# Optimization experiments

Hardware: AMD Instinct MI355X
Metric: run time of the kernel (lower is better)

The kernel has to match this reference:

```python
import jax, jax.numpy as jnp
import numpy as np

N_NODES = 100000
IN_FEATURES = 5000
OUT_FEATURES = 64
NNZ = 4000000


def setup_inputs() -> dict:
    key = jax.random.key(0)
    k_row, k_col, k_val, k_w, k_b = jax.random.split(key, 5)
    rows = jax.random.randint(k_row, (NNZ,), 0, N_NODES, dtype=jnp.int64 if jax.config.jax_enable_x64 else jnp.int32)
    cols = jax.random.randint(k_col, (NNZ,), 0, IN_FEATURES, dtype=rows.dtype)
    index = jnp.stack([rows, cols], axis=0)  # [2, nnz] COO
    value = jax.random.uniform(k_val, (NNZ,), dtype=jnp.float32)
    # kaiming_uniform_(mode='fan_out', a=sqrt(5)) on [in, out]: fan_out = out_features
    gain = np.sqrt(2.0 / (1.0 + 5.0))
    bound_w = gain * np.sqrt(3.0 / OUT_FEATURES)
    weight = jax.random.uniform(k_w, (IN_FEATURES, OUT_FEATURES), jnp.float32, -bound_w, bound_w)
    bound_b = 1.0 / np.sqrt(OUT_FEATURES)
    bias = jax.random.uniform(k_b, (OUT_FEATURES,), jnp.float32, -bound_b, bound_b)
    return {"index": index, "value": value, "n": N_NODES, "weight": weight, "bias": bias}


def reference(index, value, n, weight, bias):
    # spmm: out[r, :] = sum over nnz with row==r of value * weight[col, :]
    rows, cols = index[0], index[1]
    contrib = value[:, None] * weight[cols]            # [nnz, out] gather + scale
    res = jax.ops.segment_sum(contrib, rows, num_segments=n)  # [n, out] scatter-add
    return res + bias[None, :]
```

## Files before the change

kernel.cpp:

```cpp
#include <hip/hip_runtime.h>


#define NBF 1024
#define DMAX 128
#define CH 4096
#define CC 1536
#define SP_T 512

__global__ void k_zero1024(int* __restrict__ p) { p[threadIdx.x] = 0; }

__global__ __launch_bounds__(512) void kA_hist(const int* __restrict__ rows, int nnz,
        unsigned M, int S, int* __restrict__ hist2dF, int* __restrict__ hist2dC) {
    __shared__ int h[NBF];
    int t = threadIdx.x, blk = blockIdx.x;
    long long base = (long long)blk * CH;
    int count = (int)min((long long)CH, (long long)nnz - base);
    h[t] = 0; h[t + 512] = 0;
    __syncthreads();
#pragma unroll
    for (int k = 0; k < 8; ++k) {
        int i = t + (k << 9);
        if (i < count) {
            unsigned r = (unsigned)rows[base + i];
            int f = (int)(((unsigned long long)r * M) >> S);
            atomicAdd(&h[f], 1);
        }
    }
    __syncthreads();
    hist2dF[blk * NBF + t] = h[t];
    hist2dF[blk * NBF + 512 + t] = h[t + 512];
    if (t < 64) {
        int s = 0;
#pragma unroll
        for (int j = 0; j < 16; ++j) s += h[(t << 4) + j];
        hist2dC[(blk << 6) + t] = s;
    }
}

__global__ __launch_bounds__(1024) void kB1_reduce(const int* __restrict__ hist2dF,
        int nChunks, int* __restrict__ gcnt) {
    int t = threadIdx.x;
    int s = 0;
    for (int b = blockIdx.x; b < nChunks; b += gridDim.x) s += hist2dF[b * NBF + t];
    if (s) atomicAdd(&gcnt[t], s);
}

__global__ __launch_bounds__(1024) void kB_off(const int* __restrict__ gcnt,
        const int* __restrict__ hist2dC, int nChunks, int* __restrict__ fineBase,
        int* __restrict__ cursorF, int* __restrict__ blockOffC, int doOff) {
    __shared__ int sE[NBF];
    __shared__ int wsum[16];
    __shared__ int totalSh;
    int t = threadIdx.x, lane = t & 63, wv = t >> 6;
    int v = gcnt[t];
    int x = v;
#pragma unroll
    for (int off = 1; off < 64; off <<= 1) {
        int y = __shfl_up(x, off, 64);
        if (lane >= off) x += y;
    }
    if (lane == 63) wsum[wv] = x;
    __syncthreads();
    if (t < 16) {
        int s = wsum[t], xs = s;
#pragma unroll
        for (int off = 1; off < 16; off <<= 1) {
            int y = __shfl_up(xs, off, 16);
            if (t >= off) xs += y;
        }
        wsum[t] = xs - s;
    }
    __syncthreads();
    int incl = x + wsum[wv], excl = incl - v;
    sE[t] = excl;
    if (blockIdx.x == 0) {
        fineBase[t] = excl;
        cursorF[t] = excl;
        if (t == NBF - 1) fineBase[NBF] = incl;
    }
    __syncthreads();
    if (!doOff) return;
    int c = blockIdx.x;
    int carry = sE[c << 4];
    for (int b2 = 0; b2 < nChunks; b2 += 1024) {
        int idx = b2 + t;
        int hv = (idx < nChunks) ? hist2dC[(idx << 6) + c] : 0;
        int hx = hv;
#pragma unroll
        for (int off = 1; off < 64; off <<= 1) {
            int y = __shfl_up(hx, off, 64);
            if (lane >= off) hx += y;
        }
        if (lane == 63) wsum[wv] = hx;
        __syncthreads();
        if (t < 16) {
            int s = wsum[t], xs = s;
#pragma unroll
            for (int off = 1; off < 16; off <<= 1) {
                int y = __shfl_up(xs, off, 16);
                if (t >= off) xs += y;
            }
            wsum[t] = xs - s;
        }
        __syncthreads();
        int hincl = hx + wsum[wv];
        if (idx < nChunks) blockOffC[(idx << 6) + c] = carry + hincl - hv;
        if (t == 1023) totalSh = hincl;
        __syncthreads();
        carry += totalSh;
    }
}

__global__ void k_ghist(const int* __restrict__ rows, int nnz, unsigned M, int S,
                        int* __restrict__ gcnt) {
    __shared__ int h[NBF];
    int t = threadIdx.x;
    for (int i = t; i < NBF; i += blockDim.x) h[i] = 0;
    __syncthreads();
    for (int i = blockIdx.x * blockDim.x + t; i < nnz; i += gridDim.x * blockDim.x) {
        unsigned r = (unsigned)rows[i];
        int f = (int)(((unsigned long long)r * M) >> S);
        atomicAdd(&h[f], 1);
    }
    __syncthreads();
    for (int i = t; i < NBF; i += blockDim.x)
        if (h[i]) atomicAdd(&gcnt[i], h[i]);
}

__global__ __launch_bounds__(512) void kC_bin1(const int* __restrict__ rows,
        const int* __restrict__ cols, const float* __restrict__ vals, int nnz,
        unsigned M, int S, int d, const int* __restrict__ blockOffC,
        unsigned long long* __restrict__ pairs1) {
    __shared__ unsigned long long stage[CH];
    __shared__ int histC[64], scC[64], adjC[64];
    int t = threadIdx.x, blk = blockIdx.x;
    long long base = (long long)blk * CH;
    int count = (int)min((long long)CH, (long long)nnz - base);
    if (t < 64) histC[t] = 0;
    __syncthreads();
    int cs8[8], rk8[8];
    unsigned long long pk8[8];
#pragma unroll
    for (int k = 0; k < 8; ++k) {
        int i = t + (k << 9);
        cs8[k] = -1;
        if (i < count) {
            unsigned r = (unsigned)rows[base + i];
            int c = cols[base + i];
            float v = vals[base + i];
            int f = (int)(((unsigned long long)r * M) >> S);
            int lr = (int)r - f * d;
            int cs = f >> 4;
            cs8[k] = cs;
            rk8[k] = atomicAdd(&histC[cs], 1);
            pk8[k] = ((unsigned long long)__float_as_uint(v) << 32) |
                     ((unsigned)f << 20) | ((unsigned)lr << 13) | (unsigned)c;
        }
    }
    __syncthreads();
    if (t < 64) {
        int v = histC[t], x = v;
#pragma unroll
        for (int off = 1; off < 64; off <<= 1) {
            int y = __shfl_up(x, off, 64);
            if (t >= off) x += y;
        }
        scC[t] = x;
        adjC[t] = blockOffC[(blk << 6) + t] - (x - v);
    }
    __syncthreads();
#pragma unroll
    for (int k = 0; k < 8; ++k)
        if (cs8[k] >= 0) stage[(scC[cs8[k]] - histC[cs8[k]]) + rk8[k]] = pk8[k];
    __syncthreads();
    for (int i = t; i < count; i += 512) {
        unsigned long long p = stage[i];
        int cs = (int)((p >> 24) & 63);
        pairs1[adjC[cs] + i] = p;
    }
}

__global__ __launch_bounds__(1024) void kD_bin2(const unsigned long long* __restrict__ pairs1,
        int nnz, int* __restrict__ cursorF, unsigned long long* __restrict__ pairs2) {
    __shared__ unsigned long long stage[CH];
    __shared__ int histW[64], scW[64], adjW[64];
    __shared__ int f0sh;
    int t = threadIdx.x;
    long long base = (long long)blockIdx.x * CH;
    int count = (int)min((long long)CH, (long long)nnz - base);
    if (t == 0) {
        int fFirst = (int)((pairs1[base] >> 20) & 1023);
        int fLast  = (int)((pairs1[base + count - 1] >> 20) & 1023);
        int f0 = (fFirst >> 4) << 4;
        f0sh = (fLast < f0 + 64) ? f0 : -1;
    }
    if (t < 64) histW[t] = 0;
    __syncthreads();
    int f0 = f0sh;
    if (f0 < 0) {
#pragma unroll
        for (int k = 0; k < 4; ++k) {
            int i = t + (k << 10);
            if (i < count) {
                unsigned long long p = pairs1[base + i];
                int f = (int)((p >> 20) & 1023);
                int pos = atomicAdd(&cursorF[f], 1);
                pairs2[pos] = p;
            }
        }
        return;
    }
    int k4[4], rk4[4];
    unsigned long long pk4[4];
#pragma unroll
    for (int k = 0; k < 4; ++k) {
        int i = t + (k << 10);
        k4[k] = -1;
        if (i < count) {
            unsigned long long p = pairs1[base + i];
            int kf = (int)((p >> 20) & 1023) - f0;
            k4[k] = kf;
            rk4[k] = atomicAdd(&histW[kf], 1);
            pk4[k] = p;
        }
    }
    __syncthreads();
    if (t < 64) {
        int v = histW[t], x = v;
#pragma unroll
        for (int off = 1; off < 64; off <<= 1) {
            int y = __shfl_up(x, off, 64);
            if (t >= off) x += y;
        }
        scW[t] = x;
        if (v > 0) {
            int g = atomicAdd(&cursorF[f0 + t], v);
            adjW[t] = g - (x - v);
        }
    }
    __syncthreads();
#pragma unroll
    for (int k = 0; k < 4; ++k)
        if (k4[k] >= 0) stage[(scW[k4[k]] - histW[k4[k]]) + rk4[k]] = pk4[k];
    __syncthreads();
    for (int i = t; i < count; i += 1024) {
        unsigned long long p = stage[i];
        int kf = (int)((p >> 20) & 1023) - f0;
        pairs2[adjW[kf] + i] = p;
    }
}

__global__ __launch_bounds__(1024) void k_bin_direct(const int* __restrict__ rows,
        const int* __restrict__ cols, const float* __restrict__ vals, int nnz,
        unsigned M, int S, int d, int* __restrict__ cursorF,
        unsigned long long* __restrict__ pairs1) {
    __shared__ unsigned long long stage[CH];
    __shared__ int histF[NBF], scF[NBF], adjF[NBF];
    __shared__ int wsum[16];
    int t = threadIdx.x, lane = t & 63, wv = t >> 6;
    long long base = (long long)blockIdx.x * CH;
    int count = (int)min((long long)CH, (long long)nnz - base);
    histF[t] = 0;
    __syncthreads();
    int f4[4], rk4[4];
    unsigned long long pk4[4];
#pragma unroll
    for (int k = 0; k < 4; ++k) {
        int i = t + (k << 10);
        f4[k] = -1;
        if (i < count) {
            unsigned r = (unsigned)rows[base + i];
            int c = cols[base + i];
            float vv = vals[base + i];
            int f = (int)(((unsigned long long)r * M) >> S);
            int lr = (int)r - f * d;
            f4[k] = f;
            rk4[k] = atomicAdd(&histF[f], 1);
            pk4[k] = ((unsigned long long)__float_as_uint(vv) << 32) |
                     ((unsigned)f << 20) | ((unsigned)lr << 13) | (unsigned)c;
        }
    }
    __syncthreads();
    int v = histF[t], x = v;
#pragma unroll
    for (int off = 1; off < 64; off <<= 1) {
        int y = __shfl_up(x, off, 64);
        if (lane >= off) x += y;
    }
    if (lane == 63) wsum[wv] = x;
    __syncthreads();
    if (t < 16) {
        int s = wsum[t], xs = s;
#pragma unroll
        for (int off = 1; off < 16; off <<= 1) {
            int y = __shfl_up(xs, off, 16);
            if (t >= off) xs += y;
        }
        wsum[t] = xs - s;
    }
    __syncthreads();
    int incl = x + wsum[wv];
    scF[t] = incl;
    if (v > 0) {
        int g = atomicAdd(&cursorF[t], v);
        adjF[t] = g - (incl - v);
    }
    __syncthreads();
#pragma unroll
    for (int k = 0; k < 4; ++k)
        if (f4[k] >= 0) stage[(scF[f4[k]] - histF[f4[k]]) + rk4[k]] = pk4[k];
    __syncthreads();
    for (int i = t; i < count; i += 1024) {
        unsigned long long p = stage[i];
        int f = (int)((p >> 20) & 1023);
        pairs1[adjF[f] + i] = p;
    }
}

__global__ __launch_bounds__(SP_T, 8) void k_spmm5(
        const unsigned long long* __restrict__ pairs, const int* __restrict__ fineBase,
        const float* __restrict__ weight, const float* __restrict__ bias,
        float* __restrict__ out, int d, int n) {
    __shared__ unsigned long long stage[CC];
    __shared__ int histR[DMAX], scR[DMAX];
    extern __shared__ float acc[];
    int b = blockIdx.x, t = threadIdx.x;
    int row0 = b * d;
    if (row0 >= n) return;
    int nrows = min(d, n - row0);
    int start = fineBase[b], end = fineBase[b + 1];

    for (int i = t; i < (nrows << 6); i += SP_T) acc[i] = 0.0f;

    int g = t >> 4, fq = t & 15;
    for (int cb = start; cb < end; cb += CC) {
        int cnt = min(CC, end - cb);
        if (t < DMAX) histR[t] = 0;
        __syncthreads();
        int lr3[3], rk3[3];
        unsigned long long pk3[3];
#pragma unroll
        for (int k = 0; k < 3; ++k) {
            int i = t + (k << 9);
            lr3[k] = -1;
            if (i < cnt) {
                unsigned long long p = pairs[cb + i];
                int lr = (int)((p >> 13) & 127);
                lr3[k] = lr;
                rk3[k] = atomicAdd(&histR[lr], 1);
                pk3[k] = p;
            }
        }
        __syncthreads();
        if (t < DMAX) {
            int v = histR[t], x = v;
            int lane = t & 63;
#pragma unroll
            for (int off = 1; off < 64; off <<= 1) {
                int y = __shfl_up(x, off, 64);
                if (lane >= off) x += y;
            }
            scR[t] = x;
        }
        __syncthreads();
        if (t >= 64 && t < DMAX) scR[t] += scR[63];
        __syncthreads();
#pragma unroll
        for (int k = 0; k < 3; ++k)
            if (lr3[k] >= 0) stage[(scR[lr3[k]] - histR[lr3[k]]) + rk3[k]] = pk3[k];
        __syncthreads();

        for (int r = g; r < nrows; r += 32) {
            int e = scR[r], s = e - histR[r];
            if (s >= e) continue;
            float4 a = {0.0f, 0.0f, 0.0f, 0.0f};
            int j = s;
            for (; j + 4 <= e; j += 4) {
                unsigned long long p0 = stage[j + 0];
                unsigned long long p1 = stage[j + 1];
                unsigned long long p2 = stage[j + 2];
                unsigned long long p3 = stage[j + 3];
                const float4 w0 = *(const float4*)(weight + (((int)(p0 & 8191)) << 6) + (fq << 2));
                const float4 w1 = *(const float4*)(weight + (((int)(p1 & 8191)) << 6) + (fq << 2));
                const float4 w2 = *(const float4*)(weight + (((int)(p2 & 8191)) << 6) + (fq << 2));
                const float4 w3 = *(const float4*)(weight + (((int)(p3 & 8191)) << 6) + (fq << 2));
                float v0 = __uint_as_float((unsigned)(p0 >> 32));
                float v1 = __uint_as_float((unsigned)(p1 >> 32));
                float v2 = __uint_as_float((unsigned)(p2 >> 32));
                float v3 = __uint_as_float((unsigned)(p3 >> 32));
                a.x = fmaf(v0, w0.x, a.x); a.y = fmaf(v0, w0.y, a.y);
                a.z = fmaf(v0, w0.z, a.z); a.w = fmaf(v0, w0.w, a.w);
                a.x = fmaf(v1, w1.x, a.x); a.y = fmaf(v1, w1.y, a.y);
                a.z = fmaf(v1, w1.z, a.z); a.w = fmaf(v1, w1.w, a.w);
                a.x = fmaf(v2, w2.x, a.x); a.y = fmaf(v2, w2.y, a.y);
                a.z = fmaf(v2, w2.z, a.z); a.w = fmaf(v2, w2.w, a.w);
                a.x = fmaf(v3, w3.x, a.x); a.y = fmaf(v3, w3.y, a.y);
                a.z = fmaf(v3, w3.z, a.z); a.w = fmaf(v3, w3.w, a.w);
            }
            for (; j < e; ++j) {
                unsigned long long p = stage[j];
                float vv = __uint_as_float((unsigned)(p >> 32));
                const float4 w = *(const float4*)(weight + (((int)(p & 8191)) << 6) + (fq << 2));
                a.x = fmaf(vv, w.x, a.x); a.y = fmaf(vv, w.y, a.y);
                a.z = fmaf(vv, w.z, a.z); a.w = fmaf(vv, w.w, a.w);
            }
            float4* ap = (float4*)&acc[(r << 6) + (fq << 2)];
            float4 o = *ap;
            o.x += a.x; o.y += a.y; o.z += a.z; o.w += a.w;
            *ap = o;
        }
        __syncthreads();
    }

    for (int i = t; i < (nrows << 6); i += SP_T)
        out[((long long)row0 << 6) + i] = acc[i] + bias[i & 63];
}

extern "C" void kernel_launch(void* const* d_in, const int* in_sizes, int n_in,
                              void* d_out, int out_size, void* d_ws, size_t ws_size,
                              hipStream_t stream) {
    const int*   index  = (const int*)d_in[0];
    const float* value  = (const float*)d_in[1];
    const float* weight = (const float*)d_in[3];
    const float* bias   = (const float*)d_in[4];
    float*       out    = (float*)d_out;

    int nnz = in_sizes[0] / 2;
    int n   = out_size / 64;
    const int* rows = index;
    const int* cols = index + nnz;

    int d = (n + NBF - 1) / NBF;
    unsigned M = 0;
    int S = 0;
    for (S = 20; S <= 40; ++S) {
        unsigned long long m = ((1ull << S) + (unsigned)d - 1) / (unsigned)d;
        unsigned long long e = m * (unsigned long long)d - (1ull << S);
        if (m <= 0xffffffffull && e * (unsigned long long)(n > 0 ? n - 1 : 0) < (1ull << S)) {
            M = (unsigned)m;
            break;
        }
    }

    int nChunks = (nnz + CH - 1) / CH;
    char* ws = (char*)d_ws;
    int* fineBase = (int*)ws;
    int* cursorF  = (int*)(ws + (8 << 10));
    int* gcnt     = (int*)(ws + (12 << 10));
    size_t offC = 64 << 10;
    size_t szC  = (((size_t)nChunks * 64 * 4) + 255) & ~(size_t)255;
    size_t offO = offC + szC;
    size_t offF = offO + szC;
    size_t szF  = (((size_t)nChunks * NBF * 4) + 255) & ~(size_t)255;
    size_t offP1 = offF + szF;
    size_t szP   = (((size_t)nnz * 8) + 255) & ~(size_t)255;
    size_t offP2 = offP1 + szP;
    int* hist2dC   = (int*)(ws + offC);
    int* blockOffC = (int*)(ws + offO);
    int* hist2dF   = (int*)(ws + offF);
    unsigned long long* pairs1 = (unsigned long long*)(ws + offP1);
    unsigned long long* pairs2 = (unsigned long long*)(ws + offP2);
    unsigned long long* pairs3 = (unsigned long long*)(ws + offC);

    bool two = ws_size >= offP2 + szP;
    bool dir = !two && ws_size >= offP1 + szP;

    k_zero1024<<<1, 1024, 0, stream>>>(gcnt);
    size_t smem = (size_t)d * 64 * sizeof(float);
    if (two || dir) {
        kA_hist<<<nChunks, 512, 0, stream>>>(rows, nnz, M, S, hist2dF, hist2dC);
        kB1_reduce<<<64, 1024, 0, stream>>>(hist2dF, nChunks, gcnt);
        if (two) {
            kB_off<<<64, 1024, 0, stream>>>(gcnt, hist2dC, nChunks, fineBase, cursorF,
                                            blockOffC, 1);
            kC_bin1<<<nChunks, 512, 0, stream>>>(rows, cols, value, nnz, M, S, d,
                                                 blockOffC, pairs1);
            kD_bin2<<<nChunks, 1024, 0, stream>>>(pairs1, nnz, cursorF, pairs2);
            k_spmm5<<<NBF, SP_T, smem, stream>>>(pairs2, fineBase, weight, bias, out, d, n);
        } else {
            kB_off<<<1, 1024, 0, stream>>>(gcnt, hist2dC, nChunks, fineBase, cursorF,
                                           blockOffC, 0);
            k_bin_direct<<<nChunks, 1024, 0, stream>>>(rows, cols, value, nnz, M, S, d,
                                                       cursorF, pairs1);
            k_spmm5<<<NBF, SP_T, smem, stream>>>(pairs1, fineBase, weight, bias, out, d, n);
        }
    } else {
        k_ghist<<<256, 512, 0, stream>>>(rows, nnz, M, S, gcnt);
        kB_off<<<1, 1024, 0, stream>>>(gcnt, hist2dC, nChunks, fineBase, cursorF,
                                       blockOffC, 0);
        k_bin_direct<<<nChunks, 1024, 0, stream>>>(rows, cols, value, nnz, M, S, d,
                                                   cursorF, pairs3);
        k_spmm5<<<NBF, SP_T, smem, stream>>>(pairs3, fineBase, weight, bias, out, d, n);
    }
}
```

Measured before the change: 186.7 us.

## Prefetch next pair chunk, balance rows via shared ticket, drop atomic histogram reduce

The SpMM kernel now loads the next chunk of (row, col, value) pairs into registers while the current chunk is being staged and consumed, so global-load latency is hidden behind compute. Rows are handed to 16-lane groups through a shared atomic ticket instead of a fixed stride, which evens out work when row lengths differ. The histogram reduce now writes each column's total directly from a shared-memory partial sum across 16 blocks, removing the global atomics and the separate zeroing launch on the main path. The costs are extra registers for the prefetch buffer and a shared atomic plus a lane shuffle for every row.

Result: slower. 196.9 us (+5.5%).

```diff
diff --git a/kernel.cpp b/kernel.cpp
--- a/kernel.cpp
+++ b/kernel.cpp
@@ -37,12 +37,22 @@
     }
 }
 
-__global__ __launch_bounds__(1024) void kB1_reduce(const int* __restrict__ hist2dF,
+__global__ __launch_bounds__(1024) void kB1b(const int* __restrict__ hist2dF,
         int nChunks, int* __restrict__ gcnt) {
+    __shared__ int part[16][64];
     int t = threadIdx.x;
+    int col = (blockIdx.x << 6) + (t & 63);
+    int cg = t >> 6;
     int s = 0;
-    for (int b = blockIdx.x; b < nChunks; b += gridDim.x) s += hist2dF[b * NBF + t];
-    if (s) atomicAdd(&gcnt[t], s);
+    for (int ch = cg; ch < nChunks; ch += 16) s += hist2dF[ch * NBF + col];
+    part[cg][t & 63] = s;
+    __syncthreads();
+    if (t < 64) {
+        int sum = 0;
+#pragma unroll
+        for (int k = 0; k < 16; ++k) sum += part[k][t];
+        gcnt[(blockIdx.x << 6) + t] = sum;
+    }
 }
 
 __global__ __launch_bounds__(1024) void kB_off(const int* __restrict__ gcnt,
@@ -317,12 +327,13 @@
     }
 }
 
-__global__ __launch_bounds__(SP_T, 8) void k_spmm5(
+__global__ __launch_bounds__(SP_T, 8) void k_spmm6(
         const unsigned long long* __restrict__ pairs, const int* __restrict__ fineBase,
         const float* __restrict__ weight, const float* __restrict__ bias,
         float* __restrict__ out, int d, int n) {
     __shared__ unsigned long long stage[CC];
     __shared__ int histR[DMAX], scR[DMAX];
+    __shared__ int ticket;
     extern __shared__ float acc[];
     int b = blockIdx.x, t = threadIdx.x;
     int row0 = b * d;
@@ -332,29 +343,42 @@
 
     for (int i = t; i < (nrows << 6); i += SP_T) acc[i] = 0.0f;
 
-    int g = t >> 4, fq = t & 15;
-    for (int cb = start; cb < end; cb += CC) {
+    int lane = t & 63, fq = t & 15;
+    int gfirst = lane & ~15;
+
+    unsigned long long pk3[3];
+    int cb = start;
+    {
+        int cnt0 = min(CC, end - cb);
+#pragma unroll
+        for (int k = 0; k < 3; ++k) {
+            int i = t + (k << 9);
+            pk3[k] = (i < cnt0) ? pairs[cb + i] : 0ull;
+        }
+    }
+
+    while (cb < end) {
         int cnt = min(CC, end - cb);
         if (t < DMAX) histR[t] = 0;
+        if (t == 0) ticket = 0;
         __syncthreads();
         int lr3[3], rk3[3];
-        unsigned long long pk3[3];
+        unsigned long long cur3[3];
 #pragma unroll
         for (int k = 0; k < 3; ++k) {
             int i = t + (k << 9);
             lr3[k] = -1;
             if (i < cnt) {
-                unsigned long long p = pairs[cb + i];
+                unsigned long long p = pk3[k];
                 int lr = (int)((p >> 13) & 127);
                 lr3[k] = lr;
                 rk3[k] = atomicAdd(&histR[lr], 1);
-                pk3[k] = p;
+                cur3[k] = p;
             }
         }
         __syncthreads();
         if (t < DMAX) {
             int v = histR[t], x = v;
-            int lane = t & 63;
 #pragma unroll
             for (int off = 1; off < 64; off <<= 1) {
                 int y = __shfl_up(x, off, 64);
@@ -367,10 +391,25 @@
         __syncthreads();
 #pragma unroll
         for (int k = 0; k < 3; ++k)
-            if (lr3[k] >= 0) stage[(scR[lr3[k]] - histR[lr3[k]]) + rk3[k]] = pk3[k];
-        __syncthreads();
-
-        for (int r = g; r < nrows; r += 32) {
+            if (lr3[k] >= 0) stage[(scR[lr3[k]] - histR[lr3[k]]) + rk3[k]] = cur3[k];
+
+        int ncb = cb + CC;
+        if (ncb < end) {
+            int ncnt = min(CC, end - ncb);
+#pragma unroll
+            for (int k = 0; k < 3; ++k) {
+                int i = t + (k << 9);
+                pk3[k] = (i < ncnt) ? pairs[ncb + i] : 0ull;
+            }
+        }
+        __syncthreads();
+
+        for (;;) {
+            int tk = 0;
+            if ((t & 15) == 0) tk = atomicAdd(&ticket, 1);
+            tk = __shfl(tk, gfirst, 64);
+            if (tk >= nrows) break;
+            int r = tk;
             int e = scR[r], s = e - histR[r];
             if (s >= e) continue;
             float4 a = {0.0f, 0.0f, 0.0f, 0.0f};
@@ -409,6 +448,7 @@
             o.x += a.x; o.y += a.y; o.z += a.z; o.w += a.w;
             *ap = o;
         }
+        cb = ncb;
         __syncthreads();
     }
 
@@ -465,31 +505,31 @@
     bool two = ws_size >= offP2 + szP;
     bool dir = !two && ws_size >= offP1 + szP;
 
-    k_zero1024<<<1, 1024, 0, stream>>>(gcnt);
     size_t smem = (size_t)d * 64 * sizeof(float);
     if (two || dir) {
         kA_hist<<<nChunks, 512, 0, stream>>>(rows, nnz, M, S, hist2dF, hist2dC);
-        kB1_reduce<<<64, 1024, 0, stream>>>(hist2dF, nChunks, gcnt);
+        kB1b<<<16, 1024, 0, stream>>>(hist2dF, nChunks, gcnt);
         if (two) {
             kB_off<<<64, 1024, 0, stream>>>(gcnt, hist2dC, nChunks, fineBase, cursorF,
                                             blockOffC, 1);
             kC_bin1<<<nChunks, 512, 0, stream>>>(rows, cols, value, nnz, M, S, d,
                                                  blockOffC, pairs1);
             kD_bin2<<<nChunks, 1024, 0, stream>>>(pairs1, nnz, cursorF, pairs2);
-            k_spmm5<<<NBF, SP_T, smem, stream>>>(pairs2, fineBase, weight, bias, out, d, n);
+            k_spmm6<<<NBF, SP_T, smem, stream>>>(pairs2, fineBase, weight, bias, out, d, n);
         } else {
             kB_off<<<1, 1024, 0, stream>>>(gcnt, hist2dC, nChunks, fineBase, cursorF,
                                            blockOffC, 0);
             k_bin_direct<<<nChunks, 1024, 0, stream>>>(rows, cols, value, nnz, M, S, d,
                                                        cursorF, pairs1);
-            k_spmm5<<<NBF, SP_T, smem, stream>>>(pairs1, fineBase, weight, bias, out, d, n);
+            k_spmm6<<<NBF, SP_T, smem, stream>>>(pairs1, fineBase, weight, bias, out, d, n);
         }
     } else {
+        k_zero1024<<<1, 1024, 0, stream>>>(gcnt);
         k_ghist<<<256, 512, 0, stream>>>(rows, nnz, M, S, gcnt);
         kB_off<<<1, 1024, 0, stream>>>(gcnt, hist2dC, nChunks, fineBase, cursorF,
                                        blockOffC, 0);
         k_bin_direct<<<nChunks, 1024, 0, stream>>>(rows, cols, value, nnz, M, S, d,
                                                    cursorF, pairs3);
-        k_spmm5<<<NBF, SP_T, smem, stream>>>(pairs3, fineBase, weight, bias, out, d, n);
-    }
-}
+        k_spmm6<<<NBF, SP_T, smem, stream>>>(pairs3, fineBase, weight, bias, out, d, n);
+    }
+}
```
